# Kernel tuning notes

Hardware: AMD Instinct MI355X
Metric: run time of the kernel (lower is better)

Reference implementation:

```python
import jax, jax.numpy as jnp
import numpy as np

LN_EPS = 1e-5

def _layernorm(x, gamma, beta):
    mu = jnp.mean(x, axis=-1, keepdims=True)
    var = jnp.var(x, axis=-1, keepdims=True)
    return (x - mu) * jax.lax.rsqrt(var + LN_EPS) * gamma + beta

def setup_inputs() -> dict:
    key = jax.random.key(0)
    ks = jax.random.split(key, 4)
    B, s, d, L = 8, 192, 512, 8
    h = 2048  # embed_dim * 2
    return {
        "lags": jax.random.normal(ks[0], (B, s, d, L), dtype=jnp.float32),
        "gamma1": jnp.ones((d,), jnp.float32),
        "beta1": jnp.zeros((d,), jnp.float32),
        "W1": jax.random.normal(ks[1], (d, h), jnp.float32) * (1.0 / np.sqrt(d)),
        "b1": jnp.zeros((h,), jnp.float32),
        "W2": jax.random.normal(ks[2], (h, d), jnp.float32) * (1.0 / np.sqrt(h)),
        "b2": jnp.zeros((d,), jnp.float32),
        "gamma3": jnp.ones((d,), jnp.float32),
        "beta3": jnp.zeros((d,), jnp.float32),
    }

def reference(lags, gamma1, beta1, W1, b1, W2, b2, gamma3, beta3):
    B, s, d, L = lags.shape
    # (B, s, d, L) -> (B, s, L, d) -> (B, S=s*L, d)
    x = jnp.transpose(lags, (0, 1, 3, 2)).reshape(B, s * L, d)
    scale = 1.0 / jnp.sqrt(jnp.asarray(d, x.dtype))
    # single-head, unprojected attention: scores = X X^T / sqrt(d)
    scores = jnp.einsum('bqd,bkd->bqk', x, x) * scale  # [B, S, S]
    attn = jax.nn.softmax(scores, axis=-1)
    attn_out = jnp.einsum('bqk,bkd->bqd', attn, x)
    q = _layernorm(x + attn_out, gamma1, beta1)
    ff = jnp.dot(jax.nn.gelu(jnp.dot(q, W1) + b1, approximate=False), W2) + b2
    out = _layernorm(q + ff, gamma3, beta3)
    # (B, S, d) -> (B, s, L, d) -> (B, s, d, L)
    return jnp.transpose(out.reshape(B, s, L, d), (0, 1, 3, 2))
```

## Files before the change

kernel.cpp:

```cpp
#include <hip/hip_runtime.h>
#include <hip/hip_bf16.h>
#include <math.h>

#define B_ 8
#define S_ 192
#define D_ 512
#define L_ 8
#define SQ 1536
#define H_ 2048
#define NROW (B_*SQ)
#define SCALE_QK 0.04419417382415922f

typedef unsigned short ushort_t;
typedef unsigned int uint_t;
typedef __attribute__((ext_vector_type(8))) short bf16x8;
typedef __attribute__((ext_vector_type(4))) float f32x4;

__device__ __forceinline__ float bfu2f(ushort_t u) { return __uint_as_float((unsigned)u << 16); }
__device__ __forceinline__ ushort_t f2bfu(float f) {
  __hip_bfloat16 h = __float2bfloat16(f);
  return *reinterpret_cast<ushort_t*>(&h);
}

__device__ __forceinline__ size_t pidx(int row, int k, int R) {
  return ((size_t)(k >> 6) * R + row) * 64 + ((((k >> 3) & 7) ^ (row & 7)) << 3) + (k & 7);
}

__device__ __forceinline__ float gelu_fast(float x) {
  float z = fabsf(x) * 0.70710678118654752f;
  float t = __builtin_amdgcn_rcpf(fmaf(0.3275911f, z, 1.0f));
  float p = fmaf(1.061405429f, t, -1.453152027f);
  p = fmaf(p, t, 1.421413741f);
  p = fmaf(p, t, -0.284496736f);
  p = fmaf(p, t, 0.254829592f);
  p = p * t;
  float e = __expf(-z * z);
  float erfz = fmaf(-p, e, 1.0f);
  float s = (x >= 0.0f) ? erfz : -erfz;
  return 0.5f * x * (1.0f + s);
}

__device__ __forceinline__ void gl_lds16(const ushort_t* g, ushort_t* l) {
  __builtin_amdgcn_global_load_lds(
      (const __attribute__((address_space(1))) unsigned int*)g,
      (__attribute__((address_space(3))) unsigned int*)l, 16, 0, 0);
}

__global__ __launch_bounds__(256) void k_build_x_f(const float* __restrict__ lags,
                                                   float* __restrict__ x,
                                                   ushort_t* __restrict__ x_bf) {
  __shared__ float tile[512][9];
  const int tid = threadIdx.x;
  const float* in = lags + (size_t)blockIdx.x * 4096;
  #pragma unroll
  for (int it = 0; it < 4; ++it) {
    int f = (tid + it * 256) * 4;
    float4 v = *reinterpret_cast<const float4*>(in + f);
    int k = f >> 3, l0 = f & 7;
    tile[k][l0] = v.x; tile[k][l0 + 1] = v.y; tile[k][l0 + 2] = v.z; tile[k][l0 + 3] = v.w;
  }
  __syncthreads();
  const int l = tid >> 5, kbase = tid & 31;
  const int r = blockIdx.x * 8 + l;
  const int b = r / SQ, rloc = r - b * SQ;
  ushort_t* xb = x_bf + (size_t)b * SQ * D_;
  #pragma unroll
  for (int j = 0; j < 16; ++j) {
    int k = kbase + 32 * j;
    float v = tile[k][l];
    x[(size_t)r * D_ + k] = v;
    xb[pidx(rloc, k, SQ)] = f2bfu(v);
  }
}

__global__ __launch_bounds__(256) void k_xt(const ushort_t* __restrict__ x_bf,
                                            ushort_t* __restrict__ xT) {
  __shared__ ushort_t tile[64][65];
  int t0 = blockIdx.x * 64, d0 = blockIdx.y * 64;
  const ushort_t* X = x_bf + (size_t)blockIdx.z * SQ * D_;
  ushort_t* XT = xT + (size_t)blockIdx.z * SQ * D_;
  for (int i = threadIdx.x; i < 4096; i += 256) {
    int tt = i >> 6, dd = i & 63;
    tile[dd][tt] = X[pidx(t0 + tt, d0 + dd, SQ)];
  }
  __syncthreads();
  for (int i = threadIdx.x; i < 4096; i += 256) {
    int dd = i >> 6, tt = i & 63;
    XT[pidx(d0 + dd, t0 + tt, D_)] = tile[dd][tt];
  }
}

__global__ __launch_bounds__(256) void k_wt(const float* __restrict__ W,
                                            ushort_t* __restrict__ Wt,
                                            int K, int N) {
  __shared__ ushort_t tile[64][65];
  int n0 = blockIdx.x * 64, k0 = blockIdx.y * 64;
  for (int i = threadIdx.x; i < 4096; i += 256) {
    int kk = i >> 6, nn = i & 63;
    tile[nn][kk] = f2bfu(W[(size_t)(k0 + kk) * N + n0 + nn]);
  }
  __syncthreads();
  for (int i = threadIdx.x; i < 4096; i += 256) {
    int nn = i >> 6, kk = i & 63;
    Wt[pidx(n0 + nn, k0 + kk, N)] = tile[nn][kk];
  }
}

template<int MODE>
__global__ __launch_bounds__(256) void k_gemm(const ushort_t* __restrict__ A,
                                              const ushort_t* __restrict__ Bt,
                                              const float* __restrict__ bias,
                                              void* __restrict__ Cout,
                                              int M, int K, int N,
                                              size_t sAz, size_t sBz, size_t sCz,
                                              float scale) {
  A  += (size_t)blockIdx.z * sAz;
  Bt += (size_t)blockIdx.z * sBz;
  __shared__ ushort_t As[128 * 64];
  __shared__ ushort_t Bs[128 * 64];
  const int tid = threadIdx.x;
  const int m0 = blockIdx.y * 128, n0 = blockIdx.x * 128;
  const int w = tid >> 6, lane = tid & 63;
  const int wr = w >> 1, wc = w & 1;
  const int l15 = lane & 15, quad = lane >> 4;
  const int xsw = l15 & 7;
  ushort_t* lA = &As[(w * 32) * 64];
  ushort_t* lB = &Bs[(w * 32) * 64];

  f32x4 acc[4][4];
  if (MODE <= 1) {
    #pragma unroll
    for (int nj = 0; nj < 4; ++nj) {
      float bv = bias[n0 + wc * 64 + nj * 16 + l15];
      #pragma unroll
      for (int mi = 0; mi < 4; ++mi) acc[mi][nj] = (f32x4){bv, bv, bv, bv};
    }
  } else {
    #pragma unroll
    for (int nj = 0; nj < 4; ++nj)
      #pragma unroll
      for (int mi = 0; mi < 4; ++mi) acc[mi][nj] = (f32x4){0.f, 0.f, 0.f, 0.f};
  }

  const int NT = K >> 6;
  for (int t = 0; t < NT; ++t) {
    const ushort_t* gA = A  + ((size_t)t * M + m0 + w * 32) * 64 + lane * 8;
    const ushort_t* gB = Bt + ((size_t)t * N + n0 + w * 32) * 64 + lane * 8;
    __syncthreads();
    #pragma unroll
    for (int j = 0; j < 4; ++j) {
      gl_lds16(gA + j * 512, lA + j * 512);
      gl_lds16(gB + j * 512, lB + j * 512);
    }
    __syncthreads();
    #pragma unroll
    for (int kk = 0; kk < 2; ++kk) {
      const int csel = ((kk * 4 + quad) ^ xsw) * 8;
      bf16x8 af[4], bfv[4];
      #pragma unroll
      for (int mi = 0; mi < 4; ++mi)
        af[mi] = *reinterpret_cast<const bf16x8*>(&As[(wr * 64 + mi * 16 + l15) * 64 + csel]);
      #pragma unroll
      for (int nj = 0; nj < 4; ++nj)
        bfv[nj] = *reinterpret_cast<const bf16x8*>(&Bs[(wc * 64 + nj * 16 + l15) * 64 + csel]);
      #pragma unroll
      for (int mi = 0; mi < 4; ++mi)
        #pragma unroll
        for (int nj = 0; nj < 4; ++nj)
          acc[mi][nj] = __builtin_amdgcn_mfma_f32_16x16x32_bf16(af[mi], bfv[nj], acc[mi][nj], 0, 0, 0);
    }
  }

  ushort_t* Cb = (ushort_t*)Cout + (size_t)blockIdx.z * sCz;
  float*    Cf = (float*)Cout    + (size_t)blockIdx.z * sCz;
  #pragma unroll
  for (int mi = 0; mi < 4; ++mi)
    #pragma unroll
    for (int nj = 0; nj < 4; ++nj) {
      int gc = n0 + wc * 64 + nj * 16 + l15;
      #pragma unroll
      for (int r = 0; r < 4; ++r) {
        int gr = m0 + wr * 64 + mi * 16 + quad * 4 + r;
        float v = acc[mi][nj][r];
        if (MODE == 0) {
          Cb[pidx(gr, gc, M)] = f2bfu(gelu_fast(v));
        } else if (MODE == 1) {
          Cf[(size_t)gr * N + gc] = v;
        } else if (MODE == 2) {
          Cb[pidx(gr, gc, M)] = f2bfu(v * scale);
        } else {
          Cf[(size_t)gr * N + gc] = v;
        }
      }
    }
}

__global__ __launch_bounds__(256) void k_softmax_bf(ushort_t* __restrict__ sc) {
  ushort_t* base = sc + (size_t)blockIdx.z * SQ * SQ;
  const int r = blockIdx.x;
  int tid = threadIdx.x;
  __shared__ float red[8];
  uint_t addr[3];
  float v[6];
  float m = -1e30f;
  #pragma unroll
  for (int j = 0; j < 3; ++j) {
    int k2 = 2 * tid + 512 * j;
    addr[j] = (uint_t)(pidx(r, k2, SQ) >> 1);
    uint_t u = ((uint_t*)base)[addr[j]];
    v[2*j]   = __uint_as_float(u << 16);
    v[2*j+1] = __uint_as_float(u & 0xffff0000u);
    m = fmaxf(m, fmaxf(v[2*j], v[2*j+1]));
  }
  #pragma unroll
  for (int o = 32; o > 0; o >>= 1) m = fmaxf(m, __shfl_down(m, o));
  if ((tid & 63) == 0) red[tid >> 6] = m;
  __syncthreads();
  m = fmaxf(fmaxf(red[0], red[1]), fmaxf(red[2], red[3]));
  __syncthreads();
  float ssum = 0.f;
  #pragma unroll
  for (int k = 0; k < 6; ++k) { v[k] = expf(v[k] - m); ssum += v[k]; }
  #pragma unroll
  for (int o = 32; o > 0; o >>= 1) ssum += __shfl_down(ssum, o);
  if ((tid & 63) == 0) red[4 + (tid >> 6)] = ssum;
  __syncthreads();
  float inv = 1.0f / (red[4] + red[5] + red[6] + red[7]);
  #pragma unroll
  for (int j = 0; j < 3; ++j) {
    uint_t lo = f2bfu(v[2*j] * inv);
    uint_t hi = f2bfu(v[2*j+1] * inv);
    ((uint_t*)base)[addr[j]] = (hi << 16) | lo;
  }
}

__global__ __launch_bounds__(256) void k_ln1b(const float* __restrict__ x,
                                              const float* __restrict__ attn,
                                              const float* __restrict__ g,
                                              const float* __restrict__ be,
                                              ushort_t* __restrict__ qbf) {
  const int row = blockIdx.x;
  size_t base = (size_t)row * D_;
  int tid = threadIdx.x;
  __shared__ float rl[8];
  float v0 = x[base + tid] + attn[base + tid];
  float v1 = x[base + tid + 256] + attn[base + tid + 256];
  float s = v0 + v1, sq = v0 * v0 + v1 * v1;
  #pragma unroll
  for (int o = 32; o > 0; o >>= 1) { s += __shfl_down(s, o); sq += __shfl_down(sq, o); }
  int lane = tid & 63, wid = tid >> 6;
  if (lane == 0) { rl[wid] = s; rl[4 + wid] = sq; }
  __syncthreads();
  s = rl[0] + rl[1] + rl[2] + rl[3];
  sq = rl[4] + rl[5] + rl[6] + rl[7];
  float mean = s * (1.0f / 512.0f);
  float var = sq * (1.0f / 512.0f) - mean * mean;
  float rstd = rsqrtf(var + 1e-5f);
  qbf[pidx(row, tid, NROW)]       = f2bfu((v0 - mean) * rstd * g[tid] + be[tid]);
  qbf[pidx(row, tid + 256, NROW)] = f2bfu((v1 - mean) * rstd * g[tid + 256] + be[tid + 256]);
}

__global__ __launch_bounds__(256) void k_ln3_f(const float* __restrict__ y,
                                               const ushort_t* __restrict__ qbf,
                                               const float* __restrict__ g3,
                                               const float* __restrict__ be3,
                                               float* __restrict__ out) {
  __shared__ float ynorm[8][512];
  const int tid = threadIdx.x;
  const int w = tid >> 6, lane = tid & 63;
  #pragma unroll
  for (int rr = 0; rr < 2; ++rr) {
    int l = 2 * w + rr;
    int t = blockIdx.x * 8 + l;
    float v[8];
    float s = 0.f, sq = 0.f;
    #pragma unroll
    for (int j = 0; j < 8; ++j) {
      int k = lane + 64 * j;
      v[j] = y[(size_t)t * D_ + k] + bfu2f(qbf[pidx(t, k, NROW)]);
      s += v[j]; sq += v[j] * v[j];
    }
    #pragma unroll
    for (int o = 32; o > 0; o >>= 1) { s += __shfl_down(s, o); sq += __shfl_down(sq, o); }
    s = __shfl(s, 0); sq = __shfl(sq, 0);
    float mean = s * (1.0f / 512.0f);
    float var = sq * (1.0f / 512.0f) - mean * mean;
    float rstd = rsqrtf(var + 1e-5f);
    #pragma unroll
    for (int j = 0; j < 8; ++j) {
      int k = lane + 64 * j;
      ynorm[l][k] = (v[j] - mean) * rstd * g3[k] + be3[k];
    }
  }
  __syncthreads();
  float* ob = out + (size_t)blockIdx.x * 4096;
  #pragma unroll
  for (int kk = 0; kk < 2; ++kk) {
    int k = tid * 2 + kk;
    float4 lo = make_float4(ynorm[0][k], ynorm[1][k], ynorm[2][k], ynorm[3][k]);
    float4 hi = make_float4(ynorm[4][k], ynorm[5][k], ynorm[6][k], ynorm[7][k]);
    *reinterpret_cast<float4*>(ob + (size_t)k * 8)     = lo;
    *reinterpret_cast<float4*>(ob + (size_t)k * 8 + 4) = hi;
  }
}

#define TS 64
#define KT 16
__global__ __launch_bounds__(256) void k_build_x_s(const float* __restrict__ lags,
                                                   float* __restrict__ x, int b_base) {
  int idx = blockIdx.x * 256 + threadIdx.x;
  int k = idx & (D_ - 1);
  int r = idx >> 9;
  int b = b_base + r / SQ;
  int t = r - (r / SQ) * SQ;
  int si = t >> 3, l = t & 7;
  size_t src = (((size_t)(b * S_ + si) * D_ + k) << 3) + l;
  x[idx] = lags[src];
}

__global__ __launch_bounds__(256) void k_scores(const float* __restrict__ x,
                                                float* __restrict__ sc, int b_base) {
  const float* A = x;
  float* C = sc;
  __shared__ float As[TS][KT + 1];
  __shared__ float Bs[TS][KT + 1];
  int tx = threadIdx.x & 15, ty = threadIdx.x >> 4;
  int j0 = blockIdx.x * TS, i0 = blockIdx.y * TS;
  float acc[4][4] = {};
  int lk = threadIdx.x & 15, lr = threadIdx.x >> 4;
  for (int k0 = 0; k0 < D_; k0 += KT) {
    #pragma unroll
    for (int it = 0; it < 4; ++it) {
      As[lr + 16 * it][lk] = A[(size_t)(i0 + lr + 16 * it) * D_ + k0 + lk];
      Bs[lr + 16 * it][lk] = A[(size_t)(j0 + lr + 16 * it) * D_ + k0 + lk];
    }
    __syncthreads();
    #pragma unroll
    for (int kk = 0; kk < KT; ++kk) {
      float a[4], bb[4];
      #pragma unroll
      for (int r = 0; r < 4; ++r) a[r] = As[ty * 4 + r][kk];
      #pragma unroll
      for (int c = 0; c < 4; ++c) bb[c] = Bs[tx * 4 + c][kk];
      #pragma unroll
      for (int r = 0; r < 4; ++r)
        #pragma unroll
        for (int c = 0; c < 4; ++c) acc[r][c] = fmaf(a[r], bb[c], acc[r][c]);
    }
    __syncthreads();
  }
  #pragma unroll
  for (int r = 0; r < 4; ++r) {
    float4 v = make_float4(acc[r][0]*SCALE_QK, acc[r][1]*SCALE_QK,
                           acc[r][2]*SCALE_QK, acc[r][3]*SCALE_QK);
    *reinterpret_cast<float4*>(&C[(size_t)(i0 + ty*4 + r) * SQ + j0 + tx*4]) = v;
  }
}

__global__ __launch_bounds__(256) void k_softmax(float* __restrict__ sc) {
  float* row = sc + (size_t)blockIdx.x * SQ;
  int tid = threadIdx.x;
  __shared__ float red[8];
  float m = -1e30f;
  for (int j = tid; j < SQ; j += 256) m = fmaxf(m, row[j]);
  #pragma unroll
  for (int o = 32; o > 0; o >>= 1) m = fmaxf(m, __shfl_down(m, o));
  if ((tid & 63) == 0) red[tid >> 6] = m;
  __syncthreads();
  m = fmaxf(fmaxf(red[0], red[1]), fmaxf(red[2], red[3]));
  __syncthreads();
  float ssum = 0.f;
  for (int j = tid; j < SQ; j += 256) { float e = expf(row[j] - m); row[j] = e; ssum += e; }
  #pragma unroll
  for (int o = 32; o > 0; o >>= 1) ssum += __shfl_down(ssum, o);
  if ((tid & 63) == 0) red[4 + (tid >> 6)] = ssum;
  __syncthreads();
  float inv = 1.0f / (red[4] + red[5] + red[6] + red[7]);
  for (int j = tid; j < SQ; j += 256) row[j] *= inv;
}

__global__ __launch_bounds__(256) void k_attn(const float* __restrict__ x,
                                              const float* __restrict__ sc,
                                              float* __restrict__ attn) {
  const float* X = x;
  const float* P = sc;
  float* O = attn;
  __shared__ float Ps[TS][KT + 1];
  __shared__ float Xs[KT][TS];
  int tx = threadIdx.x & 15, ty = threadIdx.x >> 4;
  int j0 = blockIdx.x * TS, i0 = blockIdx.y * TS;
  float acc[4][4] = {};
  int lk = threadIdx.x & 15, lr = threadIdx.x >> 4;
  int lc = threadIdx.x & 63, lrow = threadIdx.x >> 6;
  for (int k0 = 0; k0 < SQ; k0 += KT) {
    #pragma unroll
    for (int it = 0; it < 4; ++it)
      Ps[lr + 16 * it][lk] = P[(size_t)(i0 + lr + 16 * it) * SQ + k0 + lk];
    #pragma unroll
    for (int it = 0; it < 4; ++it)
      Xs[lrow + 4 * it][lc] = X[(size_t)(k0 + lrow + 4 * it) * D_ + j0 + lc];
    __syncthreads();
    #pragma unroll
    for (int kk = 0; kk < KT; ++kk) {
      float a[4], bb[4];
      #pragma unroll
      for (int r = 0; r < 4; ++r) a[r] = Ps[ty * 4 + r][kk];
      #pragma unroll
      for (int c = 0; c < 4; ++c) bb[c] = Xs[kk][tx * 4 + c];
      #pragma unroll
      for (int r = 0; r < 4; ++r)
        #pragma unroll
        for (int c = 0; c < 4; ++c) acc[r][c] = fmaf(a[r], bb[c], acc[r][c]);
    }
    __syncthreads();
  }
  #pragma unroll
  for (int r = 0; r < 4; ++r) {
    float4 v = make_float4(acc[r][0], acc[r][1], acc[r][2], acc[r][3]);
    *reinterpret_cast<float4*>(&O[(size_t)(i0 + ty*4 + r) * D_ + j0 + tx*4]) = v;
  }
}

__global__ __launch_bounds__(256) void k_ln1(const float* __restrict__ x,
                                             const float* __restrict__ attn,
                                             const float* __restrict__ g,
                                             const float* __restrict__ be,
                                             float* __restrict__ qout) {
  size_t base = (size_t)blockIdx.x * D_;
  int tid = threadIdx.x;
  __shared__ float rl[8];
  float v0 = x[base + tid] + attn[base + tid];
  float v1 = x[base + tid + 256] + attn[base + tid + 256];
  float s = v0 + v1, sq = v0 * v0 + v1 * v1;
  #pragma unroll
  for (int o = 32; o > 0; o >>= 1) { s += __shfl_down(s, o); sq += __shfl_down(sq, o); }
  int lane = tid & 63, wid = tid >> 6;
  if (lane == 0) { rl[wid] = s; rl[4 + wid] = sq; }
  __syncthreads();
  s = rl[0] + rl[1] + rl[2] + rl[3];
  sq = rl[4] + rl[5] + rl[6] + rl[7];
  float mean = s * (1.0f / 512.0f);
  float var = sq * (1.0f / 512.0f) - mean * mean;
  float rstd = rsqrtf(var + 1e-5f);
  qout[base + tid]       = (v0 - mean) * rstd * g[tid] + be[tid];
  qout[base + tid + 256] = (v1 - mean) * rstd * g[tid + 256] + be[tid + 256];
}

__global__ __launch_bounds__(256, 2) void k_ffn(
    const float* __restrict__ q,
    const float* __restrict__ W1, const float* __restrict__ b1,
    const float* __restrict__ W2, const float* __restrict__ b2,
    const float* __restrict__ g3, const float* __restrict__ be3,
    float* __restrict__ out, int row_base)
{
  __shared__ float qs[8][D_];
  __shared__ float mid[8][H_];
  const int tid = threadIdx.x;
  const int row0 = blockIdx.x * 8;
  for (int idx = tid; idx < 8 * D_; idx += 256)
    qs[idx >> 9][idx & (D_ - 1)] = q[(size_t)row0 * D_ + idx];
  __syncthreads();
  float acc[8][8];
  {
    float4 bA = *reinterpret_cast<const float4*>(b1 + (tid << 3));
    float4 bB = *reinterpret_cast<const float4*>(b1 + (tid << 3) + 4);
    float bv[8] = {bA.x, bA.y, bA.z, bA.w, bB.x, bB.y, bB.z, bB.w};
    #pragma unroll
    for (int jj = 0; jj < 8; ++jj)
      #pragma unroll
      for (int r = 0; r < 8; ++r) acc[jj][r] = bv[jj];
  }
  for (int k4 = 0; k4 < D_ / 4; ++k4) {
    float4 qv[8];
    #pragma unroll
    for (int r = 0; r < 8; ++r)
      qv[r] = *reinterpret_cast<const float4*>(&qs[r][k4 << 2]);
    #pragma unroll
    for (int kk = 0; kk < 4; ++kk) {
      const int k = (k4 << 2) + kk;
      float4 wA = *reinterpret_cast<const float4*>(W1 + (size_t)k * H_ + (tid << 3));
      float4 wB = *reinterpret_cast<const float4*>(W1 + (size_t)k * H_ + (tid << 3) + 4);
      float wv[8] = {wA.x, wA.y, wA.z, wA.w, wB.x, wB.y, wB.z, wB.w};
      #pragma unroll
      for (int r = 0; r < 8; ++r) {
        float qk = (kk == 0) ? qv[r].x : (kk == 1) ? qv[r].y : (kk == 2) ? qv[r].z : qv[r].w;
        #pragma unroll
        for (int jj = 0; jj < 8; ++jj) acc[jj][r] = fmaf(qk, wv[jj], acc[jj][r]);
      }
    }
  }
  #pragma unroll
  for (int jj = 0; jj < 8; ++jj)
    #pragma unroll
    for (int r = 0; r < 8; ++r) {
      float v = acc[jj][r];
      mid[r][(tid << 3) + jj] = 0.5f * v * (1.0f + erff(v * 0.70710678118654752f));
    }
  __syncthreads();
  float acc2[8][2];
  {
    float b20 = b2[tid << 1], b21 = b2[(tid << 1) + 1];
    #pragma unroll
    for (int r = 0; r < 8; ++r) { acc2[r][0] = b20; acc2[r][1] = b21; }
  }
  for (int j4 = 0; j4 < H_ / 4; ++j4) {
    float4 mv[8];
    #pragma unroll
    for (int r = 0; r < 8; ++r)
      mv[r] = *reinterpret_cast<const float4*>(&mid[r][j4 << 2]);
    #pragma unroll
    for (int kk = 0; kk < 4; ++kk) {
      const int j = (j4 << 2) + kk;
      float2 wv = *reinterpret_cast<const float2*>(W2 + (size_t)j * D_ + (tid << 1));
      #pragma unroll
      for (int r = 0; r < 8; ++r) {
        float m = (kk == 0) ? mv[r].x : (kk == 1) ? mv[r].y : (kk == 2) ? mv[r].z : mv[r].w;
        acc2[r][0] = fmaf(m, wv.x, acc2[r][0]);
        acc2[r][1] = fmaf(m, wv.y, acc2[r][1]);
      }
    }
  }
  __syncthreads();
  float* ys = &mid[0][0];
  #pragma unroll
  for (int r = 0; r < 8; ++r) {
    ys[r * D_ + (tid << 1)]     = qs[r][(tid << 1)]     + acc2[r][0];
    ys[r * D_ + (tid << 1) + 1] = qs[r][(tid << 1) + 1] + acc2[r][1];
  }
  __syncthreads();
  float g3a = g3[tid],  g3b = g3[tid + 256];
  float be3a = be3[tid], be3b = be3[tid + 256];
  float* rl = &qs[0][0];
  for (int r = 0; r < 8; ++r) {
    float v0 = ys[r * D_ + tid], v1 = ys[r * D_ + tid + 256];
    float s = v0 + v1, sq = v0 * v0 + v1 * v1;
    #pragma unroll
    for (int o = 32; o > 0; o >>= 1) { s += __shfl_down(s, o); sq += __shfl_down(sq, o); }
    int lane = tid & 63, wid = tid >> 6;
    if (lane == 0) { rl[wid] = s; rl[4 + wid] = sq; }
    __syncthreads();
    s = rl[0] + rl[1] + rl[2] + rl[3];
    sq = rl[4] + rl[5] + rl[6] + rl[7];
    __syncthreads();
    float mean = s * (1.0f / 512.0f);
    float var = sq * (1.0f / 512.0f) - mean * mean;
    float rstd = rsqrtf(var + 1e-5f);
    int t = row_base + row0 + r;
    int b = t / SQ, tt = t - b * SQ;
    int si = tt >> 3, l = tt & 7;
    size_t ob = (((size_t)(b * S_ + si) * D_) << 3) + l;
    out[ob + ((size_t)tid << 3)]         = (v0 - mean) * rstd * g3a + be3a;
    out[ob + ((size_t)(tid + 256) << 3)] = (v1 - mean) * rstd * g3b + be3b;
  }
}

extern "C" void kernel_launch(void* const* d_in, const int* in_sizes, int n_in,
                              void* d_out, int out_size, void* d_ws, size_t ws_size,
                              hipStream_t stream) {
  const float* lags   = (const float*)d_in[0];
  const float* gamma1 = (const float*)d_in[1];
  const float* beta1  = (const float*)d_in[2];
  const float* W1     = (const float*)d_in[3];
  const float* b1     = (const float*)d_in[4];
  const float* W2     = (const float*)d_in[5];
  const float* b2     = (const float*)d_in[6];
  const float* g3     = (const float*)d_in[7];
  const float* be3    = (const float*)d_in[8];
  float* out = (float*)d_out;

  float* ws = (float*)d_ws;
  const size_t NX  = (size_t)B_ * SQ * D_;
  const size_t NXB = (size_t)SQ * D_;
  const size_t NS  = (size_t)SQ * SQ;

  const size_t need_full = (3 * NX + 8 * NS) * sizeof(float);

  if (ws_size >= need_full) {
    float* x        = ws;
    float* attn     = x + NX;
    ushort_t* q_bf  = (ushort_t*)(attn + NX);
    ushort_t* w1t   = q_bf + NX;
    ushort_t* w2t   = w1t + (size_t)H_ * D_;
    ushort_t* region = w2t + (size_t)H_ * D_;
    ushort_t* sc_bf = region;
    ushort_t* x_bf  = region + 8 * NS;
    ushort_t* xT_bf = x_bf + NX;
    ushort_t* mid_bf = region;

    k_build_x_f<<<dim3(B_ * S_), 256, 0, stream>>>(lags, x, x_bf);
    k_xt<<<dim3(SQ / 64, D_ / 64, B_), 256, 0, stream>>>(x_bf, xT_bf);
    k_wt<<<dim3(H_ / 64, D_ / 64), 256, 0, stream>>>(W1, w1t, D_, H_);
    k_wt<<<dim3(D_ / 64, H_ / 64), 256, 0, stream>>>(W2, w2t, H_, D_);
    k_gemm<2><<<dim3(SQ / 128, SQ / 128, B_), 256, 0, stream>>>(
        x_bf, x_bf, nullptr, sc_bf, SQ, D_, SQ, NXB, NXB, NS, SCALE_QK);
    k_softmax_bf<<<dim3(SQ, 1, B_), 256, 0, stream>>>(sc_bf);
    k_gemm<3><<<dim3(D_ / 128, SQ / 128, B_), 256, 0, stream>>>(
        sc_bf, xT_bf, nullptr, attn, SQ, SQ, D_, NS, NXB, NXB, 1.0f);
    k_ln1b<<<dim3(NROW), 256, 0, stream>>>(x, attn, gamma1, beta1, q_bf);
    k_gemm<0><<<dim3(H_ / 128, NROW / 128, 1), 256, 0, stream>>>(
        q_bf, w1t, b1, mid_bf, NROW, D_, H_, 0, 0, 0, 1.0f);
    k_gemm<1><<<dim3(D_ / 128, NROW / 128, 1), 256, 0, stream>>>(
        mid_bf, w2t, b2, attn, NROW, H_, D_, 0, 0, 0, 1.0f);
    k_ln3_f<<<dim3(B_ * S_), 256, 0, stream>>>(attn, q_bf, g3, be3, out);
  } else {
    float* xb   = ws;
    float* sc   = xb + NXB;
    float* atb  = sc + NS;
    float* qb   = atb + NXB;
    for (int b = 0; b < B_; ++b) {
      k_build_x_s<<<dim3((unsigned)(NXB / 256)), 256, 0, stream>>>(lags, xb, b);
      k_scores<<<dim3(SQ / TS, SQ / TS, 1), 256, 0, stream>>>(xb, sc, b);
      k_softmax<<<dim3(SQ, 1, 1), 256, 0, stream>>>(sc);
      k_attn<<<dim3(D_ / TS, SQ / TS, 1), 256, 0, stream>>>(xb, sc, atb);
      k_ln1<<<dim3(SQ), 256, 0, stream>>>(xb, atb, gamma1, beta1, qb);
      k_ffn<<<dim3(SQ / 8), 256, 0, stream>>>(qb, W1, b1, W2, b2, g3, be3, out, b * SQ);
    }
  }
}
```

Before: 315.7 us.

## Split-K the attention-value and FFN down-projection GEMMs into two partials

Adds a split-K GEMM kernel and uses it for the attn@X GEMM (2 K-splits, bf16 partials in packed layout) and the W2 GEMM (2 K-splits, fp32 partials). The partial sums are added inside the following layernorm kernels. This raises the block count on the N=512 GEMMs, which otherwise launch few tiles, and so improves CU occupancy. The cost is extra partial-output traffic, and the attention partials are now rounded to bf16, which lowers precision.

Result: faster. 307.4 us (-2.6%).

```diff
diff --git a/kernel.cpp b/kernel.cpp
--- a/kernel.cpp
+++ b/kernel.cpp
@@ -195,6 +195,95 @@
     }
 }
 
+template<int MODE>
+__global__ __launch_bounds__(256) void k_gemm_sk(const ushort_t* __restrict__ A,
+                                                 const ushort_t* __restrict__ Bt,
+                                                 const float* __restrict__ bias,
+                                                 void* __restrict__ Cout,
+                                                 int M, int ktiles, int N, int nb,
+                                                 size_t sAz, size_t sBz,
+                                                 size_t sCz, size_t sKz,
+                                                 float scale) {
+  const int z = blockIdx.z;
+  const int b = z % nb, ks = z / nb;
+  A  += (size_t)b * sAz + (size_t)ks * ktiles * M * 64;
+  Bt += (size_t)b * sBz + (size_t)ks * ktiles * N * 64;
+  __shared__ ushort_t As[128 * 64];
+  __shared__ ushort_t Bs[128 * 64];
+  const int tid = threadIdx.x;
+  const int m0 = blockIdx.y * 128, n0 = blockIdx.x * 128;
+  const int w = tid >> 6, lane = tid & 63;
+  const int wr = w >> 1, wc = w & 1;
+  const int l15 = lane & 15, quad = lane >> 4;
+  const int xsw = l15 & 7;
+  ushort_t* lA = &As[(w * 32) * 64];
+  ushort_t* lB = &Bs[(w * 32) * 64];
+
+  f32x4 acc[4][4];
+  if (MODE <= 1 && ks == 0) {
+    #pragma unroll
+    for (int nj = 0; nj < 4; ++nj) {
+      float bv = bias[n0 + wc * 64 + nj * 16 + l15];
+      #pragma unroll
+      for (int mi = 0; mi < 4; ++mi) acc[mi][nj] = (f32x4){bv, bv, bv, bv};
+    }
+  } else {
+    #pragma unroll
+    for (int nj = 0; nj < 4; ++nj)
+      #pragma unroll
+      for (int mi = 0; mi < 4; ++mi) acc[mi][nj] = (f32x4){0.f, 0.f, 0.f, 0.f};
+  }
+
+  for (int t = 0; t < ktiles; ++t) {
+    const ushort_t* gA = A  + ((size_t)t * M + m0 + w * 32) * 64 + lane * 8;
+    const ushort_t* gB = Bt + ((size_t)t * N + n0 + w * 32) * 64 + lane * 8;
+    __syncthreads();
+    #pragma unroll
+    for (int j = 0; j < 4; ++j) {
+      gl_lds16(gA + j * 512, lA + j * 512);
+      gl_lds16(gB + j * 512, lB + j * 512);
+    }
+    __syncthreads();
+    #pragma unroll
+    for (int kk = 0; kk < 2; ++kk) {
+      const int csel = ((kk * 4 + quad) ^ xsw) * 8;
+      bf16x8 af[4], bfv[4];
+      #pragma unroll
+      for (int mi = 0; mi < 4; ++mi)
+        af[mi] = *reinterpret_cast<const bf16x8*>(&As[(wr * 64 + mi * 16 + l15) * 64 + csel]);
+      #pragma unroll
+      for (int nj = 0; nj < 4; ++nj)
+        bfv[nj] = *reinterpret_cast<const bf16x8*>(&Bs[(wc * 64 + nj * 16 + l15) * 64 + csel]);
+      #pragma unroll
+      for (int mi = 0; mi < 4; ++mi)
+        #pragma unroll
+        for (int nj = 0; nj < 4; ++nj)
+          acc[mi][nj] = __builtin_amdgcn_mfma_f32_16x16x32_bf16(af[mi], bfv[nj], acc[mi][nj], 0, 0, 0);
+    }
+  }
+
+  ushort_t* Cb = (ushort_t*)Cout + (size_t)b * sCz + (size_t)ks * sKz;
+  float*    Cf = (float*)Cout    + (size_t)b * sCz + (size_t)ks * sKz;
+  #pragma unroll
+  for (int mi = 0; mi < 4; ++mi)
+    #pragma unroll
+    for (int nj = 0; nj < 4; ++nj) {
+      int gc = n0 + wc * 64 + nj * 16 + l15;
+      #pragma unroll
+      for (int r = 0; r < 4; ++r) {
+        int gr = m0 + wr * 64 + mi * 16 + quad * 4 + r;
+        float v = acc[mi][nj][r];
+        if (MODE == 1) {
+          Cf[(size_t)gr * N + gc] = v;
+        } else if (MODE == 2) {
+          Cb[pidx(gr, gc, M)] = f2bfu(v * scale);
+        } else {
+          Cf[(size_t)gr * N + gc] = v;
+        }
+      }
+    }
+}
+
 __global__ __launch_bounds__(256) void k_softmax_bf(ushort_t* __restrict__ sc) {
   ushort_t* base = sc + (size_t)blockIdx.z * SQ * SQ;
   const int r = blockIdx.x;
@@ -235,16 +324,20 @@
 }
 
 __global__ __launch_bounds__(256) void k_ln1b(const float* __restrict__ x,
-                                              const float* __restrict__ attn,
+                                              const ushort_t* __restrict__ p,
                                               const float* __restrict__ g,
                                               const float* __restrict__ be,
                                               ushort_t* __restrict__ qbf) {
   const int row = blockIdx.x;
+  const int b = row / SQ, rloc = row - b * SQ;
+  const size_t NXu = (size_t)NROW * D_;
   size_t base = (size_t)row * D_;
   int tid = threadIdx.x;
   __shared__ float rl[8];
-  float v0 = x[base + tid] + attn[base + tid];
-  float v1 = x[base + tid + 256] + attn[base + tid + 256];
+  size_t pa0 = (size_t)b * SQ * D_ + pidx(rloc, tid, SQ);
+  size_t pa1 = (size_t)b * SQ * D_ + pidx(rloc, tid + 256, SQ);
+  float v0 = x[base + tid]       + bfu2f(p[pa0]) + bfu2f(p[NXu + pa0]);
+  float v1 = x[base + tid + 256] + bfu2f(p[pa1]) + bfu2f(p[NXu + pa1]);
   float s = v0 + v1, sq = v0 * v0 + v1 * v1;
   #pragma unroll
   for (int o = 32; o > 0; o >>= 1) { s += __shfl_down(s, o); sq += __shfl_down(sq, o); }
@@ -260,7 +353,8 @@
   qbf[pidx(row, tid + 256, NROW)] = f2bfu((v1 - mean) * rstd * g[tid + 256] + be[tid + 256]);
 }
 
-__global__ __launch_bounds__(256) void k_ln3_f(const float* __restrict__ y,
+__global__ __launch_bounds__(256) void k_ln3_f(const float* __restrict__ y0,
+                                               const float* __restrict__ y1,
                                                const ushort_t* __restrict__ qbf,
                                                const float* __restrict__ g3,
                                                const float* __restrict__ be3,
@@ -277,7 +371,7 @@
     #pragma unroll
     for (int j = 0; j < 8; ++j) {
       int k = lane + 64 * j;
-      v[j] = y[(size_t)t * D_ + k] + bfu2f(qbf[pidx(t, k, NROW)]);
+      v[j] = y0[(size_t)t * D_ + k] + y1[(size_t)t * D_ + k] + bfu2f(qbf[pidx(t, k, NROW)]);
       s += v[j]; sq += v[j] * v[j];
     }
     #pragma unroll
@@ -576,9 +670,10 @@
   const size_t need_full = (3 * NX + 8 * NS) * sizeof(float);
 
   if (ws_size >= need_full) {
-    float* x        = ws;
-    float* attn     = x + NX;
-    ushort_t* q_bf  = (ushort_t*)(attn + NX);
+    float* y0       = ws;
+    float* y1       = ws + NX;
+    ushort_t* p_bf  = (ushort_t*)y1;
+    ushort_t* q_bf  = (ushort_t*)(ws + 2 * NX);
     ushort_t* w1t   = q_bf + NX;
     ushort_t* w2t   = w1t + (size_t)H_ * D_;
     ushort_t* region = w2t + (size_t)H_ * D_;
@@ -586,6 +681,7 @@
     ushort_t* x_bf  = region + 8 * NS;
     ushort_t* xT_bf = x_bf + NX;
     ushort_t* mid_bf = region;
+    float* x = y0;
 
     k_build_x_f<<<dim3(B_ * S_), 256, 0, stream>>>(lags, x, x_bf);
     k_xt<<<dim3(SQ / 64, D_ / 64, B_), 256, 0, stream>>>(x_bf, xT_bf);
@@ -594,14 +690,14 @@
     k_gemm<2><<<dim3(SQ / 128, SQ / 128, B_), 256, 0, stream>>>(
         x_bf, x_bf, nullptr, sc_bf, SQ, D_, SQ, NXB, NXB, NS, SCALE_QK);
     k_softmax_bf<<<dim3(SQ, 1, B_), 256, 0, stream>>>(sc_bf);
-    k_gemm<3><<<dim3(D_ / 128, SQ / 128, B_), 256, 0, stream>>>(
-        sc_bf, xT_bf, nullptr, attn, SQ, SQ, D_, NS, NXB, NXB, 1.0f);
-    k_ln1b<<<dim3(NROW), 256, 0, stream>>>(x, attn, gamma1, beta1, q_bf);
+    k_gemm_sk<2><<<dim3(D_ / 128, SQ / 128, B_ * 2), 256, 0, stream>>>(
+        sc_bf, xT_bf, nullptr, p_bf, SQ, 12, D_, B_, NS, NXB, NXB, NX, 1.0f);
+    k_ln1b<<<dim3(NROW), 256, 0, stream>>>(x, p_bf, gamma1, beta1, q_bf);
     k_gemm<0><<<dim3(H_ / 128, NROW / 128, 1), 256, 0, stream>>>(
         q_bf, w1t, b1, mid_bf, NROW, D_, H_, 0, 0, 0, 1.0f);
-    k_gemm<1><<<dim3(D_ / 128, NROW / 128, 1), 256, 0, stream>>>(
-        mid_bf, w2t, b2, attn, NROW, H_, D_, 0, 0, 0, 1.0f);
-    k_ln3_f<<<dim3(B_ * S_), 256, 0, stream>>>(attn, q_bf, g3, be3, out);
+    k_gemm_sk<1><<<dim3(D_ / 128, NROW / 128, 2), 256, 0, stream>>>(
+        mid_bf, w2t, b2, y0, NROW, 16, D_, 1, 0, 0, 0, NX, 1.0f);
+    k_ln3_f<<<dim3(B_ * S_), 256, 0, stream>>>(y0, y1, q_bf, g3, be3, out);
   } else {
     float* xb   = ws;
     float* sc   = xb + NXB;
```
